# Performance work log

Hardware: AMD Instinct MI355X
Metric: run time of the kernel (lower is better)

The kernel has to match this reference:

```python
import jax, jax.numpy as jnp
import numpy as np

BATCH = 4096
DIM = 128
TEMP = 0.5

def setup_inputs() -> dict:
    key = jax.random.key(0)
    k1, k2 = jax.random.split(key)
    proj_1 = jax.random.normal(k1, (BATCH, DIM), dtype=jnp.float32)
    proj_2 = jax.random.normal(k2, (BATCH, DIM), dtype=jnp.float32)
    return {"proj_1": proj_1, "proj_2": proj_2}

def _l2norm(x, eps=1e-12):
    # matches F.normalize(p=2, dim=1)
    n = jnp.sqrt(jnp.sum(x * x, axis=1, keepdims=True))
    return x / jnp.maximum(n, eps)

def reference(proj_1, proj_2):
    B = proj_1.shape[0]
    z_i = _l2norm(proj_1)
    z_j = _l2norm(proj_2)
    reps = jnp.concatenate([z_i, z_j], axis=0)          # [2B, D]
    # cosine similarity of normalized vectors == dot product; (2B,D)x(D,2B) matmul
    sim = reps @ reps.T                                 # [2B, 2B]
    sim_ij = jnp.einsum('bd,bd->b', z_i, z_j)           # diag(sim, +B)
    sim_ji = sim_ij                                     # diag(sim, -B) is symmetric
    positives = jnp.concatenate([sim_ij, sim_ji], axis=0)  # [2B]
    nominator = jnp.exp(positives / TEMP)
    mask = (~jnp.eye(2 * B, dtype=bool)).astype(sim.dtype)
    denominator = jnp.sum(mask * jnp.exp(sim / TEMP), axis=1)  # [2B]
    all_losses = -jnp.log(nominator / denominator)
    loss = jnp.sum(all_losses) / (2 * B)
    return loss
```

## Files before the change

### kernel.cpp

```cpp
#include <hip/hip_runtime.h>
#include <hip/hip_bf16.h>
#include <math.h>

#define BATCH 4096
#define DIM 128
#define TWO_B 8192
#define SCALE 1.69864374f

typedef float floatx4 __attribute__((ext_vector_type(4)));
typedef int   intx4  __attribute__((ext_vector_type(4)));
typedef long  longx2 __attribute__((ext_vector_type(2)));

__device__ __forceinline__ longx2 as_l2(intx4 v) {
    union { intx4 a; longx2 b; } u; u.a = v; return u.b;
}
__device__ __forceinline__ unsigned char to_fp8(float v) {
    return (unsigned char)(__builtin_amdgcn_cvt_pk_fp8_f32(v, v, 0, false) & 0xff);
}


__global__ __launch_bounds__(256) void norm_kernel(const float* __restrict__ p1,
                                                   const float* __restrict__ p2,
                                                   unsigned char* __restrict__ repsF,
                                                   float* __restrict__ pos,
                                                   float* __restrict__ out) {
    __shared__ unsigned char stage[2][8][64];
    int tid = threadIdx.x;
    int w = tid >> 6, l = tid & 63;
    int b0 = blockIdx.x * 4;
    int b = b0 + w;
    const float* r1 = p1 + (size_t)b * DIM;
    const float* r2 = p2 + (size_t)b * DIM;
    float x0 = r1[l], x1 = r1[l + 64];
    float y0 = r2[l], y1 = r2[l + 64];
    float s1 = x0 * x0 + x1 * x1;
    float s2 = y0 * y0 + y1 * y1;
    float s12 = x0 * y0 + x1 * y1;
    #pragma unroll
    for (int off = 32; off; off >>= 1) {
        s1  += __shfl_xor(s1, off);
        s2  += __shfl_xor(s2, off);
        s12 += __shfl_xor(s12, off);
    }
    float n1 = fmaxf(sqrtf(s1), 1e-12f);
    float n2 = fmaxf(sqrtf(s2), 1e-12f);
    float i1 = SCALE / n1;
    float i2 = SCALE / n2;

    int cc = (l >> 3) & 3;
    int inner = ((l >> 5) & 1) * 8 + (l & 7);
    stage[0][cc    ][w * 16 + inner] = to_fp8(x0 * i1);
    stage[0][cc + 4][w * 16 + inner] = to_fp8(x1 * i1);
    stage[1][cc    ][w * 16 + inner] = to_fp8(y0 * i2);
    stage[1][cc + 4][w * 16 + inner] = to_fp8(y1 * i2);

    if (l == 0) {
        pos[b] = s12 / (n1 * n2);
        if (b == 0) out[0] = 0.0f;
    }
    __syncthreads();

    int which = tid >> 7, u = tid & 127;
    int ch = u >> 4, l16 = u & 15;
    int rowbase = which ? (b0 + BATCH) : b0;
    size_t gbyte = (size_t)(rowbase >> 4) * 2048 + ch * 256 + (b0 & 15) * 16 + l16 * 4;
    *(int*)(repsF + gbyte) = ((const int*)&stage[which][ch][0])[l16];
}

__global__ __launch_bounds__(256, 3) void sim_kernel(const unsigned char* __restrict__ repsF,
                                                     float* __restrict__ part) {
    __shared__ float stage[4][64];
    int tid = threadIdx.x;
    int wid = tid >> 6, lane = tid & 63;
    int wm = wid >> 1, wn = wid & 1;
    int lr = lane & 15, q = lane >> 4;
    int r = blockIdx.y;
    int c = blockIdx.x;
    int TM, TN;
    if (c < 64 - r) { TM = r;      TN = r + c; }
    else            { TM = 63 - r; TN = TM + (c - (64 - r)); }
    if (TM == TN && wm == 1 && wn == 0) return;
    int tm = 2 * TM + wm, tn = 2 * TN + wn;
    bool diag = (tm == tn);

    const char* base = (const char*)repsF;
    int lofs = q * 256 + lr * 16;
    const char* ab = base + tm * 8192 + lofs;
    const char* bb = base + tn * 8192 + lofs;

    longx2 aF[4][2], bF[4][2];
    #pragma unroll
    for (int mi = 0; mi < 4; ++mi)
        #pragma unroll
        for (int h = 0; h < 2; ++h) {
            aF[mi][h] = as_l2(*(const intx4*)(ab + mi * 2048 + h * 1024));
            bF[mi][h] = as_l2(*(const intx4*)(bb + mi * 2048 + h * 1024));
        }

    floatx4 acc[4][4] = {};
    #pragma unroll
    for (int ck = 0; ck < 4; ++ck) {
        int h = ck >> 1, sel = ck & 1;
        #pragma unroll
        for (int mi = 0; mi < 4; ++mi)
            #pragma unroll
            for (int ni = 0; ni < 4; ++ni)
                acc[mi][ni] = __builtin_amdgcn_mfma_f32_16x16x32_fp8_fp8(
                    aF[mi][h][sel], bF[ni][h][sel], acc[mi][ni], 0, 0, 0);
    }

    float cs[4] = {0.0f, 0.0f, 0.0f, 0.0f};
    #pragma unroll
    for (int mi = 0; mi < 4; ++mi) {
        float rp[4];
        #pragma unroll
        for (int reg = 0; reg < 4; ++reg) {
            float e0 = __builtin_amdgcn_exp2f(acc[mi][0][reg]);
            float e1 = __builtin_amdgcn_exp2f(acc[mi][1][reg]);
            float e2 = __builtin_amdgcn_exp2f(acc[mi][2][reg]);
            float e3 = __builtin_amdgcn_exp2f(acc[mi][3][reg]);
            if (diag && (q * 4 + reg) == lr) {
                if (mi == 0) e0 = 0.0f;
                if (mi == 1) e1 = 0.0f;
                if (mi == 2) e2 = 0.0f;
                if (mi == 3) e3 = 0.0f;
            }
            cs[0] += e0; cs[1] += e1; cs[2] += e2; cs[3] += e3;
            rp[reg] = (e0 + e1) + (e2 + e3);
        }
        #pragma unroll
        for (int mask = 1; mask < 16; mask <<= 1)
            #pragma unroll
            for (int reg = 0; reg < 4; ++reg)
                rp[reg] += __shfl_xor(rp[reg], mask);
        if (lr == 0) {
            #pragma unroll
            for (int reg = 0; reg < 4; ++reg)
                stage[wid][mi * 16 + q * 4 + reg] = rp[reg];
        }
    }
    part[(size_t)tn * TWO_B + tm * 64 + lane] = stage[wid][lane];

    if (!diag) {
        #pragma unroll
        for (int ni = 0; ni < 4; ++ni) {
            cs[ni] += __shfl_xor(cs[ni], 16);
            cs[ni] += __shfl_xor(cs[ni], 32);
        }
        if (q == 0) {
            #pragma unroll
            for (int ni = 0; ni < 4; ++ni)
                stage[wid][ni * 16 + lr] = cs[ni];
        }
        part[(size_t)tm * TWO_B + tn * 64 + lane] = stage[wid][lane];
    }
}

__global__ __launch_bounds__(128) void reduce_kernel(const float* __restrict__ part,
                                                     const float* __restrict__ pos,
                                                     float* __restrict__ out) {
    int tid = threadIdx.x;
    int rr = blockIdx.x * 128 + tid;
    float s0 = 0.0f, s1 = 0.0f, s2 = 0.0f, s3 = 0.0f;
    #pragma unroll 8
    for (int k = 0; k < 128; k += 4) {
        s0 += part[(size_t)(k + 0) * TWO_B + rr];
        s1 += part[(size_t)(k + 1) * TWO_B + rr];
        s2 += part[(size_t)(k + 2) * TWO_B + rr];
        s3 += part[(size_t)(k + 3) * TWO_B + rr];
    }
    float v = __logf((s0 + s1) + (s2 + s3)) - 2.0f * pos[rr & (BATCH - 1)];
    #pragma unroll
    for (int off = 32; off; off >>= 1) v += __shfl_xor(v, off);
    __shared__ float sred[2];
    int lane = tid & 63, wid = tid >> 6;
    if (lane == 0) sred[wid] = v;
    __syncthreads();
    if (tid == 0)
        atomicAdd(out, (sred[0] + sred[1]) * (1.0f / TWO_B));
}

extern "C" void kernel_launch(void* const* d_in, const int* in_sizes, int n_in,
                              void* d_out, int out_size, void* d_ws, size_t ws_size,
                              hipStream_t stream) {
    const float* p1 = (const float*)d_in[0];
    const float* p2 = (const float*)d_in[1];
    float* out = (float*)d_out;

    char* ws = (char*)d_ws;
    unsigned char* repsF = (unsigned char*)ws;
    float* pos  = (float*)(ws + (size_t)TWO_B * DIM);
    float* part = pos + BATCH;

    norm_kernel<<<BATCH / 4, 256, 0, stream>>>(p1, p2, repsF, pos, out);
    sim_kernel<<<dim3(65, 32), 256, 0, stream>>>(repsF, part);
    reduce_kernel<<<TWO_B / 128, 128, 0, stream>>>(part, pos, out);
}
```

Baseline: 89.52 us.

## Make sim kernel persistent with per-wave job loop and prefetch of next tile

Replaces the 65x32 grid of sim blocks with a persistent grid of 3072 waves. Each wave loops over 64x64 tile jobs and loads the next job's fp8 fragments while the current job's MFMAs and exp reductions run. Partial sums are now written straight to global memory from selected lanes instead of going through a shared-memory stage. This is meant to hide load latency and cut launch and tail overhead, at the cost of higher register pressure and scattered narrow stores that may not coalesce well.

```diff
diff --git a/kernel.cpp b/kernel.cpp
--- a/kernel.cpp
+++ b/kernel.cpp
@@ -6,6 +6,8 @@
 #define DIM 128
 #define TWO_B 8192
 #define SCALE 1.69864374f
+#define NJOBS 8320
+#define NWAVES 3072
 
 typedef float floatx4 __attribute__((ext_vector_type(4)));
 typedef int   intx4  __attribute__((ext_vector_type(4)));
@@ -67,92 +69,119 @@
     *(int*)(repsF + gbyte) = ((const int*)&stage[which][ch][0])[l16];
 }
 
-__global__ __launch_bounds__(256, 3) void sim_kernel(const unsigned char* __restrict__ repsF,
-                                                     float* __restrict__ part) {
-    __shared__ float stage[4][64];
-    int tid = threadIdx.x;
-    int wid = tid >> 6, lane = tid & 63;
+__device__ __forceinline__ void decode_job(int j, int& tm, int& tn, bool& skip) {
+    int c = j >> 7, r = (j >> 2) & 31, wid = j & 3;
     int wm = wid >> 1, wn = wid & 1;
-    int lr = lane & 15, q = lane >> 4;
-    int r = blockIdx.y;
-    int c = blockIdx.x;
     int TM, TN;
     if (c < 64 - r) { TM = r;      TN = r + c; }
     else            { TM = 63 - r; TN = TM + (c - (64 - r)); }
-    if (TM == TN && wm == 1 && wn == 0) return;
-    int tm = 2 * TM + wm, tn = 2 * TN + wn;
-    bool diag = (tm == tn);
-
+    skip = (TM == TN) && (wm == 1) && (wn == 0);
+    tm = 2 * TM + wm;
+    tn = 2 * TN + wn;
+}
+
+__global__ __launch_bounds__(256, 3) void sim_kernel(const unsigned char* __restrict__ repsF,
+                                                     float* __restrict__ part) {
+    int tid = threadIdx.x;
+    int lane = tid & 63;
+    int w = blockIdx.x * 4 + (tid >> 6);
+    int lr = lane & 15, q = lane >> 4;
+    int lofs = q * 256 + lr * 16;
     const char* base = (const char*)repsF;
-    int lofs = q * 256 + lr * 16;
-    const char* ab = base + tm * 8192 + lofs;
-    const char* bb = base + tn * 8192 + lofs;
+
+    int tm, tn; bool skip;
+    decode_job(w, tm, tn, skip);
 
     longx2 aF[4][2], bF[4][2];
-    #pragma unroll
-    for (int mi = 0; mi < 4; ++mi)
-        #pragma unroll
-        for (int h = 0; h < 2; ++h) {
-            aF[mi][h] = as_l2(*(const intx4*)(ab + mi * 2048 + h * 1024));
-            bF[mi][h] = as_l2(*(const intx4*)(bb + mi * 2048 + h * 1024));
-        }
-
-    floatx4 acc[4][4] = {};
-    #pragma unroll
-    for (int ck = 0; ck < 4; ++ck) {
-        int h = ck >> 1, sel = ck & 1;
+    {
+        const char* ab = base + tm * 8192 + lofs;
+        const char* bb = base + tn * 8192 + lofs;
         #pragma unroll
         for (int mi = 0; mi < 4; ++mi)
             #pragma unroll
-            for (int ni = 0; ni < 4; ++ni)
-                acc[mi][ni] = __builtin_amdgcn_mfma_f32_16x16x32_fp8_fp8(
-                    aF[mi][h][sel], bF[ni][h][sel], acc[mi][ni], 0, 0, 0);
-    }
-
-    float cs[4] = {0.0f, 0.0f, 0.0f, 0.0f};
-    #pragma unroll
-    for (int mi = 0; mi < 4; ++mi) {
-        float rp[4];
+            for (int h = 0; h < 2; ++h) {
+                aF[mi][h] = as_l2(*(const intx4*)(ab + mi * 2048 + h * 1024));
+                bF[mi][h] = as_l2(*(const intx4*)(bb + mi * 2048 + h * 1024));
+            }
+    }
+
+    #pragma unroll 1
+    for (int j = w; j < NJOBS; j += NWAVES) {
+        int tmc = tm, tnc = tn;
+        bool skipc = skip;
+        bool diag = (tmc == tnc);
+
+        floatx4 acc[4][4] = {};
         #pragma unroll
-        for (int reg = 0; reg < 4; ++reg) {
-            float e0 = __builtin_amdgcn_exp2f(acc[mi][0][reg]);
-            float e1 = __builtin_amdgcn_exp2f(acc[mi][1][reg]);
-            float e2 = __builtin_amdgcn_exp2f(acc[mi][2][reg]);
-            float e3 = __builtin_amdgcn_exp2f(acc[mi][3][reg]);
-            if (diag && (q * 4 + reg) == lr) {
-                if (mi == 0) e0 = 0.0f;
-                if (mi == 1) e1 = 0.0f;
-                if (mi == 2) e2 = 0.0f;
-                if (mi == 3) e3 = 0.0f;
-            }
-            cs[0] += e0; cs[1] += e1; cs[2] += e2; cs[3] += e3;
-            rp[reg] = (e0 + e1) + (e2 + e3);
-        }
+        for (int ck = 0; ck < 4; ++ck) {
+            int h = ck >> 1, sel = ck & 1;
+            #pragma unroll
+            for (int mi = 0; mi < 4; ++mi)
+                #pragma unroll
+                for (int ni = 0; ni < 4; ++ni)
+                    acc[mi][ni] = __builtin_amdgcn_mfma_f32_16x16x32_fp8_fp8(
+                        aF[mi][h][sel], bF[ni][h][sel], acc[mi][ni], 0, 0, 0);
+        }
+
+        int jn = j + NWAVES;
+        if (jn < NJOBS) {
+            decode_job(jn, tm, tn, skip);
+            const char* ab = base + tm * 8192 + lofs;
+            const char* bb = base + tn * 8192 + lofs;
+            #pragma unroll
+            for (int mi = 0; mi < 4; ++mi)
+                #pragma unroll
+                for (int h = 0; h < 2; ++h) {
+                    aF[mi][h] = as_l2(*(const intx4*)(ab + mi * 2048 + h * 1024));
+                    bF[mi][h] = as_l2(*(const intx4*)(bb + mi * 2048 + h * 1024));
+                }
+        }
+
+        if (skipc) continue;
+
+        float cs[4] = {0.0f, 0.0f, 0.0f, 0.0f};
         #pragma unroll
-        for (int mask = 1; mask < 16; mask <<= 1)
-            #pragma unroll
-            for (int reg = 0; reg < 4; ++reg)
-                rp[reg] += __shfl_xor(rp[reg], mask);
-        if (lr == 0) {
-            #pragma unroll
-            for (int reg = 0; reg < 4; ++reg)
-                stage[wid][mi * 16 + q * 4 + reg] = rp[reg];
-        }
-    }
-    part[(size_t)tn * TWO_B + tm * 64 + lane] = stage[wid][lane];
-
-    if (!diag) {
-        #pragma unroll
-        for (int ni = 0; ni < 4; ++ni) {
-            cs[ni] += __shfl_xor(cs[ni], 16);
-            cs[ni] += __shfl_xor(cs[ni], 32);
-        }
-        if (q == 0) {
-            #pragma unroll
-            for (int ni = 0; ni < 4; ++ni)
-                stage[wid][ni * 16 + lr] = cs[ni];
-        }
-        part[(size_t)tm * TWO_B + tn * 64 + lane] = stage[wid][lane];
+        for (int mi = 0; mi < 4; ++mi) {
+            float rp[4];
+            #pragma unroll
+            for (int reg = 0; reg < 4; ++reg) {
+                float e0 = __builtin_amdgcn_exp2f(acc[mi][0][reg]);
+                float e1 = __builtin_amdgcn_exp2f(acc[mi][1][reg]);
+                float e2 = __builtin_amdgcn_exp2f(acc[mi][2][reg]);
+                float e3 = __builtin_amdgcn_exp2f(acc[mi][3][reg]);
+                if (diag && (q * 4 + reg) == lr) {
+                    if (mi == 0) e0 = 0.0f;
+                    if (mi == 1) e1 = 0.0f;
+                    if (mi == 2) e2 = 0.0f;
+                    if (mi == 3) e3 = 0.0f;
+                }
+                cs[0] += e0; cs[1] += e1; cs[2] += e2; cs[3] += e3;
+                rp[reg] = (e0 + e1) + (e2 + e3);
+            }
+            #pragma unroll
+            for (int mask = 1; mask < 16; mask <<= 1)
+                #pragma unroll
+                for (int reg = 0; reg < 4; ++reg)
+                    rp[reg] += __shfl_xor(rp[reg], mask);
+            if (lr == 0) {
+                #pragma unroll
+                for (int reg = 0; reg < 4; ++reg)
+                    part[(size_t)tnc * TWO_B + tmc * 64 + mi * 16 + q * 4 + reg] =
+                        rp[reg];
+            }
+        }
+        if (!diag) {
+            #pragma unroll
+            for (int ni = 0; ni < 4; ++ni) {
+                cs[ni] += __shfl_xor(cs[ni], 16);
+                cs[ni] += __shfl_xor(cs[ni], 32);
+            }
+            if (q == 0) {
+                #pragma unroll
+                for (int ni = 0; ni < 4; ++ni)
+                    part[(size_t)tmc * TWO_B + tnc * 64 + ni * 16 + lr] = cs[ni];
+            }
+        }
     }
 }
 
@@ -193,6 +222,6 @@
     float* part = pos + BATCH;
 
     norm_kernel<<<BATCH / 4, 256, 0, stream>>>(p1, p2, repsF, pos, out);
-    sim_kernel<<<dim3(65, 32), 256, 0, stream>>>(repsF, part);
+    sim_kernel<<<NWAVES / 4, 256, 0, stream>>>(repsF, part);
     reduce_kernel<<<TWO_B / 128, 128, 0, stream>>>(part, pos, out);
 }
```

After: 92.22 us. 1.03x slower.
